# Optimization experiments

Hardware: AMD Instinct MI355X
Metric: run time of the kernel (lower is better)

## Reference

```python
import jax, jax.numpy as jnp
import numpy as np

N, E, G, D, C = 50000, 800000, 512, 128, 10
BN_EPS = 1e-5

def setup_inputs() -> dict:
    key = jax.random.key(0)
    ks = jax.random.split(key, 12)
    inp = {
        'x': jnp.zeros((N,), dtype=jnp.int64 if jax.config.jax_enable_x64 else jnp.int32),
        'edge_index': jax.random.randint(ks[0], (2, E), 0, N),
        'batch_ids': jnp.sort(jax.random.randint(ks[1], (N,), 0, G)),
        'emb': jax.random.normal(ks[2], (1, D), jnp.float32),
        'W1a': jax.random.normal(ks[3], (D, D), jnp.float32) * 0.05,
        'b1a': jnp.zeros((D,), jnp.float32),
        'g1': jnp.ones((D,), jnp.float32),
        'be1': jnp.zeros((D,), jnp.float32),
        'W1b': jax.random.normal(ks[4], (D, D), jnp.float32) * 0.05,
        'b1b': jnp.zeros((D,), jnp.float32),
        'W2a': jax.random.normal(ks[5], (D, D), jnp.float32) * 0.05,
        'b2a': jnp.zeros((D,), jnp.float32),
        'g2': jnp.ones((D,), jnp.float32),
        'be2': jnp.zeros((D,), jnp.float32),
        'W2b': jax.random.normal(ks[6], (D, D), jnp.float32) * 0.05,
        'b2b': jnp.zeros((D,), jnp.float32),
        'Wm': jax.random.normal(ks[7], (D, C), jnp.float32) * 0.05,
        'bm': jnp.zeros((C,), jnp.float32),
        'Wx': jax.random.normal(ks[8], (D, C), jnp.float32) * 0.05,
        'bx': jnp.zeros((C,), jnp.float32),
        'ens_w': jnp.array([0.6, 0.4], jnp.float32),
    }
    return inp

def _gin_layer(h, src, dst, Wa, ba, g, be, Wb, bb):
    # GINConv, eps=0: mlp(x + sum_{j in N(i)} x_j)
    agg = jax.ops.segment_sum(h[src], dst, num_segments=N)  # [N, D]
    z = (h + agg) @ Wa + ba
    mu = jnp.mean(z, axis=0)
    var = jnp.var(z, axis=0)  # biased, as torch BN training forward
    z = (z - mu) * jax.lax.rsqrt(var + BN_EPS) * g + be
    z = jax.nn.relu(z)  # dropout is identity in eval
    return z @ Wb + bb

def reference(x, edge_index, batch_ids, emb, W1a, b1a, g1, be1, W1b, b1b,
              W2a, b2a, g2, be2, W2b, b2b, Wm, bm, Wx, bx, ens_w):
    src, dst = edge_index[0], edge_index[1]
    h0 = emb[x]  # [N, D] (all indices 0)
    h1 = _gin_layer(h0, src, dst, W1a, b1a, g1, be1, W1b, b1b)
    h2 = _gin_layer(h1, src, dst, W2a, b2a, g2, be2, W2b, b2b) + h1
    # global mean / max pooling over batch segments
    counts = jax.ops.segment_sum(jnp.ones((N,), h2.dtype), batch_ids, num_segments=G)
    mean_repr = jax.ops.segment_sum(h2, batch_ids, num_segments=G) / jnp.maximum(counts, 1.0)[:, None]
    max_repr = jax.ops.segment_max(h2, batch_ids, num_segments=G)
    max_repr = jnp.where(jnp.isfinite(max_repr), max_repr, 0.0)  # empty segments -> 0
    logits_mean = mean_repr @ Wm + bm
    logits_max = max_repr @ Wx + bx
    w = jax.nn.softmax(ens_w)
    ensemble_logits = w[0] * logits_mean + w[1] * logits_max
    return (ensemble_logits, logits_mean, logits_max, (mean_repr, max_repr))
```

## Files before the change

### kernel.cpp

```cpp
#include <hip/hip_runtime.h>
#include <math.h>

#define N_NODES  50000
#define N_EDGES  800000
#define N_GRAPHS 512
#define DIM      128
#define NCLS     10
#define KH       64
#define KW       32
#define KT       128
#define OVF_CAP  65536
#define BN_EPS   1e-5f

#define TR       32
#define NB_GEMM  ((N_NODES + TR - 1) / TR)
#define NB_EDGE  ((N_EDGES / 4 + 255) / 256)
#define NB_MID   (NB_EDGE + KT)


__global__ void k_zero(uint4* __restrict__ p, int n4) {
    int i = blockIdx.x * blockDim.x + threadIdx.x;
    if (i < n4) p[i] = make_uint4(0u, 0u, 0u, 0u);
}

__global__ void k_count_deg(const int4* __restrict__ dst4, int* __restrict__ deg,
                            uint4* __restrict__ m4) {
    int e = blockIdx.x * blockDim.x + threadIdx.x;
    const uint4 z = make_uint4(0u, 0u, 0u, 0u);
    for (int i = e; i < N_NODES * KW / 4; i += NB_EDGE * 256) m4[i] = z;
    if (e < N_EDGES / 4) {
        int4 d = dst4[e];
        atomicAdd(&deg[d.x], 1);
        atomicAdd(&deg[d.y], 1);
        atomicAdd(&deg[d.z], 1);
        atomicAdd(&deg[d.w], 1);
    }
}

__device__ inline int lower_bound_i(const int* __restrict__ a, int n, int v) {
    int lo = 0, hi = n;
    while (lo < hi) {
        int mid = (lo + hi) >> 1;
        if (a[mid] < v) lo = mid + 1; else hi = mid;
    }
    return lo;
}

__global__ __launch_bounds__(256) void k_mid(
        const int4* __restrict__ src4, const int4* __restrict__ dst4,
        const int* __restrict__ deg, unsigned int* __restrict__ m,
        unsigned int* __restrict__ ovf_cnt, int* __restrict__ ovf_buf,
        const float* __restrict__ emb, const float* __restrict__ W1a,
        const float* __restrict__ g1, const float* __restrict__ be1,
        const float* __restrict__ W1b, const float* __restrict__ b1b,
        const float* __restrict__ W2a, const float* __restrict__ b2b,
        float* __restrict__ table, float* __restrict__ table2) {
    const int t = threadIdx.x;
    if ((int)blockIdx.x < NB_EDGE) {
        int e = blockIdx.x * 256 + t;
        if (e >= N_EDGES / 4) return;
        int4 sv = src4[e];
        int4 dv = dst4[e];
        int ss[4] = {sv.x, sv.y, sv.z, sv.w};
        int dd[4] = {dv.x, dv.y, dv.z, dv.w};
        #pragma unroll
        for (int j = 0; j < 4; ++j) {
            int k = deg[ss[j]];
            if (k < KH) {
                atomicAdd(&m[(size_t)dd[j] * KW + (k >> 1)], 1u << ((k & 1) << 4));
            } else {
                unsigned int idx = atomicAdd(ovf_cnt, 1u);
                if (idx < OVF_CAP) {
                    ovf_buf[2 * idx] = dd[j];
                    ovf_buf[2 * idx + 1] = k < KT ? k : KT - 1;
                }
            }
        }
    } else {
        __shared__ unsigned long long sred[256];
        __shared__ float r[DIM];
        __shared__ float traw[DIM];
        const int k = blockIdx.x - NB_EDGE;
        unsigned long long s = 0;
        for (int i = t; i < N_NODES; i += 256) {
            unsigned long long d = (unsigned long long)(unsigned int)deg[i];
            s += d * d;
        }
        sred[t] = s;
        __syncthreads();
        for (int st = 128; st > 0; st >>= 1) {
            if (t < st) sred[t] += sred[t + st];
            __syncthreads();
        }
        if (t < DIM) {
            float u = 0.f;
            for (int j = 0; j < DIM; ++j) u += emb[j] * W1a[j * DIM + t];
            double mdeg = (double)N_EDGES / (double)N_NODES;
            double vdeg = (double)sred[0] / (double)N_NODES - mdeg * mdeg;
            float var = (float)((double)u * (double)u * vdeg);
            float rs  = rsqrtf(var + BN_EPS);
            float A   = u * rs * g1[t];
            float B   = be1[t] - (float)mdeg * A;
            r[t] = fmaxf((float)k * A + B, 0.f);
        }
        __syncthreads();
        if (t < DIM) {
            float acc = b1b[t];
            for (int j = 0; j < DIM; ++j) acc += r[j] * W1b[j * DIM + t];
            traw[t] = acc;
            table[(size_t)k * DIM + t] = acc + b2b[t];
        }
        __syncthreads();
        if (t < DIM) {
            float acc2 = 0.f;
            for (int j = 0; j < DIM; ++j) acc2 += traw[j] * W2a[j * DIM + t];
            table2[(size_t)k * DIM + t] = acc2;
        }
    }
}

__global__ __launch_bounds__(256) void k_gemm1(
        const unsigned int* __restrict__ m, const int* __restrict__ deg,
        const float* __restrict__ table2, const float* __restrict__ b2a,
        float* __restrict__ z2, float* __restrict__ spart,
        const unsigned int* __restrict__ ovf_cnt, const int* __restrict__ ovf_buf) {
    __shared__ __align__(16) float nsh[TR * 68];
    const int t = threadIdx.x;
    const int i0 = blockIdx.x * TR;
    {
        int row = t >> 3, w4 = (t & 7) << 2;
        uint4 v = make_uint4(0u, 0u, 0u, 0u);
        if (i0 + row < N_NODES) v = *(const uint4*)&m[(size_t)(i0 + row) * KW + w4];
        float* np = &nsh[row * 68 + (w4 << 1)];
        float4 f0 = make_float4((float)(v.x & 0xFFFFu), (float)(v.x >> 16),
                                (float)(v.y & 0xFFFFu), (float)(v.y >> 16));
        float4 f1 = make_float4((float)(v.z & 0xFFFFu), (float)(v.z >> 16),
                                (float)(v.w & 0xFFFFu), (float)(v.w >> 16));
        *(float4*)&np[0] = f0;
        *(float4*)&np[4] = f1;
    }
    __syncthreads();
    if (t < TR) {
        int i = i0 + t;
        if (i < N_NODES) {
            int d = deg[i];
            if (d < KH) nsh[t * 68 + d] += 1.f;
        }
    }
    __syncthreads();

    const int g = t >> 5;
    const int c4 = (t & 31) << 2;
    const int rbase = g * 4;
    float acc[4][4] = {};
    #pragma unroll 2
    for (int kb = 0; kb < 16; ++kb) {
        const int k0 = kb * 4;
        float4 w0 = *(const float4*)&table2[(size_t)(k0 + 0) * DIM + c4];
        float4 w1 = *(const float4*)&table2[(size_t)(k0 + 1) * DIM + c4];
        float4 w2 = *(const float4*)&table2[(size_t)(k0 + 2) * DIM + c4];
        float4 w3 = *(const float4*)&table2[(size_t)(k0 + 3) * DIM + c4];
        #pragma unroll
        for (int r = 0; r < 4; ++r) {
            float4 nr = *(const float4*)&nsh[(rbase + r) * 68 + k0];
            acc[r][0] += nr.x * w0.x + nr.y * w1.x + nr.z * w2.x + nr.w * w3.x;
            acc[r][1] += nr.x * w0.y + nr.y * w1.y + nr.z * w2.y + nr.w * w3.y;
            acc[r][2] += nr.x * w0.z + nr.y * w1.z + nr.z * w2.z + nr.w * w3.z;
            acc[r][3] += nr.x * w0.w + nr.y * w1.w + nr.z * w2.w + nr.w * w3.w;
        }
    }

    unsigned int nov = *ovf_cnt;
    if (nov > OVF_CAP) nov = OVF_CAP;
    for (unsigned int u = 0; u < nov; ++u) {
        int dd = ovf_buf[2 * u];
        int rr = dd - i0;
        if (rr >= 0 && rr < TR && (rr >> 2) == g) {
            int kk = ovf_buf[2 * u + 1];
            float4 tv = *(const float4*)&table2[(size_t)kk * DIM + c4];
            acc[rr & 3][0] += tv.x; acc[rr & 3][1] += tv.y;
            acc[rr & 3][2] += tv.z; acc[rr & 3][3] += tv.w;
        }
    }

    float4 bb = *(const float4*)&b2a[c4];
    float s4[4] = {0.f, 0.f, 0.f, 0.f};
    float q4[4] = {0.f, 0.f, 0.f, 0.f};
    #pragma unroll
    for (int r = 0; r < 4; ++r) {
        int row = i0 + rbase + r;
        if (row < N_NODES) {
            float v0 = acc[r][0] + bb.x;
            float v1 = acc[r][1] + bb.y;
            float v2 = acc[r][2] + bb.z;
            float v3 = acc[r][3] + bb.w;
            int kk = deg[row];
            if (kk >= KH) {
                if (kk > KT - 1) kk = KT - 1;
                float4 sv = *(const float4*)&table2[(size_t)kk * DIM + c4];
                v0 += sv.x; v1 += sv.y; v2 += sv.z; v3 += sv.w;
            }
            *(float4*)&z2[(size_t)row * DIM + c4] = make_float4(v0, v1, v2, v3);
            s4[0] += v0; q4[0] += v0 * v0;
            s4[1] += v1; q4[1] += v1 * v1;
            s4[2] += v2; q4[2] += v2 * v2;
            s4[3] += v3; q4[3] += v3 * v3;
        }
    }
    __syncthreads();
    float* red = nsh;
    #pragma unroll
    for (int j = 0; j < 4; ++j) {
        red[g * 128 + c4 + j] = s4[j];
        red[1024 + g * 128 + c4 + j] = q4[j];
    }
    __syncthreads();
    if (t < 128) {
        float ss = 0.f, qq = 0.f;
        #pragma unroll
        for (int gg = 0; gg < 8; ++gg) {
            ss += red[gg * 128 + t];
            qq += red[1024 + gg * 128 + t];
        }
        spart[(size_t)blockIdx.x * 256 + t] = ss;
        spart[(size_t)blockIdx.x * 256 + 128 + t] = qq;
    }
}

__global__ __launch_bounds__(1024) void k_fin(
        const float* __restrict__ spart,
        const float* __restrict__ g2, const float* __restrict__ be2,
        float* __restrict__ A2, float* __restrict__ B2) {
    __shared__ double red[4 * 256];
    int t = threadIdx.x & 255;
    int q = threadIdx.x >> 8;
    double acc = 0.0;
    #pragma unroll 4
    for (int b = q; b < NB_GEMM; b += 4) acc += (double)spart[(size_t)b * 256 + t];
    red[q * 256 + t] = acc;
    __syncthreads();
    if (threadIdx.x < 256)
        red[threadIdx.x] = red[threadIdx.x] + red[256 + threadIdx.x] +
                           red[512 + threadIdx.x] + red[768 + threadIdx.x];
    __syncthreads();
    if (threadIdx.x < 128) {
        double mu = red[threadIdx.x] / (double)N_NODES;
        double var = red[128 + threadIdx.x] / (double)N_NODES - mu * mu;
        float rs = rsqrtf((float)var + BN_EPS);
        float a = rs * g2[threadIdx.x];
        A2[threadIdx.x] = a;
        B2[threadIdx.x] = be2[threadIdx.x] - (float)mu * a;
    }
}

__global__ __launch_bounds__(256) void k_gemm2(
        const float* __restrict__ z2, const float* __restrict__ A2,
        const float* __restrict__ B2, const float* __restrict__ W2b,
        const float* __restrict__ table, const int* __restrict__ deg,
        float* __restrict__ h2) {
    __shared__ __align__(16) float lds_zn[TR * 132];
    const int t = threadIdx.x;
    const int i0 = blockIdx.x * TR;
    #pragma unroll
    for (int q = 0; q < 4; ++q) {
        int idx = t + 256 * q;
        int row = idx >> 5, cc = (idx & 31) << 2;
        float4 zv = make_float4(0.f, 0.f, 0.f, 0.f);
        if (i0 + row < N_NODES) zv = *(const float4*)&z2[(size_t)(i0 + row) * DIM + cc];
        float4 av = *(const float4*)&A2[cc];
        float4 bv = *(const float4*)&B2[cc];
        lds_zn[row * 132 + cc + 0] = fmaxf(zv.x * av.x + bv.x, 0.f);
        lds_zn[row * 132 + cc + 1] = fmaxf(zv.y * av.y + bv.y, 0.f);
        lds_zn[row * 132 + cc + 2] = fmaxf(zv.z * av.z + bv.z, 0.f);
        lds_zn[row * 132 + cc + 3] = fmaxf(zv.w * av.w + bv.w, 0.f);
    }
    __syncthreads();

    const int g = t >> 5;
    const int c4 = (t & 31) << 2;
    const int rbase = g * 4;
    float acc[4][4] = {};
    #pragma unroll 2
    for (int kb = 0; kb < 32; ++kb) {
        const int k0 = kb * 4;
        float4 w0 = *(const float4*)&W2b[(size_t)(k0 + 0) * DIM + c4];
        float4 w1 = *(const float4*)&W2b[(size_t)(k0 + 1) * DIM + c4];
        float4 w2 = *(const float4*)&W2b[(size_t)(k0 + 2) * DIM + c4];
        float4 w3 = *(const float4*)&W2b[(size_t)(k0 + 3) * DIM + c4];
        #pragma unroll
        for (int r = 0; r < 4; ++r) {
            float4 zr = *(const float4*)&lds_zn[(rbase + r) * 132 + k0];
            acc[r][0] += zr.x * w0.x + zr.y * w1.x + zr.z * w2.x + zr.w * w3.x;
            acc[r][1] += zr.x * w0.y + zr.y * w1.y + zr.z * w2.y + zr.w * w3.y;
            acc[r][2] += zr.x * w0.z + zr.y * w1.z + zr.z * w2.z + zr.w * w3.z;
            acc[r][3] += zr.x * w0.w + zr.y * w1.w + zr.z * w2.w + zr.w * w3.w;
        }
    }

    #pragma unroll
    for (int r = 0; r < 4; ++r) {
        int row = i0 + rbase + r;
        if (row < N_NODES) {
            int kk = deg[row]; if (kk > KT - 1) kk = KT - 1;
            float4 tb = *(const float4*)&table[(size_t)kk * DIM + c4];
            float4 o;
            o.x = acc[r][0] + tb.x;
            o.y = acc[r][1] + tb.y;
            o.z = acc[r][2] + tb.z;
            o.w = acc[r][3] + tb.w;
            *(float4*)&h2[(size_t)row * DIM + c4] = o;
        }
    }
}

__global__ __launch_bounds__(1024) void k_poolhead(
        const float* __restrict__ h2, const int* __restrict__ batch,
        const float* __restrict__ Wm, const float* __restrict__ bm,
        const float* __restrict__ Wx, const float* __restrict__ bx,
        const float* __restrict__ ensw,
        float* __restrict__ out_ens, float* __restrict__ out_lm,
        float* __restrict__ out_lx,
        float* __restrict__ out_mean, float* __restrict__ out_max) {
    __shared__ float reds[32 * 132];
    __shared__ float redm[32 * 132];
    int g = blockIdx.x;
    int s0 = lower_bound_i(batch, N_NODES, g);
    int e0 = lower_bound_i(batch, N_NODES, g + 1);
    int rg = threadIdx.x >> 5;
    int c4 = (threadIdx.x & 31) << 2;
    float s[4] = {0.f, 0.f, 0.f, 0.f};
    float mx[4] = {-INFINITY, -INFINITY, -INFINITY, -INFINITY};
    for (int i = s0 + rg; i < e0; i += 32) {
        float4 v = *(const float4*)&h2[(size_t)i * DIM + c4];
        s[0] += v.x; mx[0] = fmaxf(mx[0], v.x);
        s[1] += v.y; mx[1] = fmaxf(mx[1], v.y);
        s[2] += v.z; mx[2] = fmaxf(mx[2], v.z);
        s[3] += v.w; mx[3] = fmaxf(mx[3], v.w);
    }
    #pragma unroll
    for (int j = 0; j < 4; ++j) {
        reds[rg * 132 + c4 + j] = s[j];
        redm[rg * 132 + c4 + j] = mx[j];
    }
    __syncthreads();
    for (int step = 16; step >= 1; step >>= 1) {
        if (rg < step) {
            #pragma unroll
            for (int j = 0; j < 4; ++j) {
                reds[rg * 132 + c4 + j] += reds[(rg + step) * 132 + c4 + j];
                redm[rg * 132 + c4 + j] = fmaxf(redm[rg * 132 + c4 + j],
                                                redm[(rg + step) * 132 + c4 + j]);
            }
        }
        __syncthreads();
    }
    if (rg == 0) {
        int cnt = e0 - s0;
        float denom = (float)(cnt > 0 ? cnt : 1);
        #pragma unroll
        for (int j = 0; j < 4; ++j) {
            float mean = reds[c4 + j] / denom;
            float mxv  = (cnt > 0) ? redm[c4 + j] : 0.f;
            out_mean[(size_t)g * DIM + c4 + j] = mean;
            out_max[(size_t)g * DIM + c4 + j]  = mxv;
            reds[c4 + j] = mean;
            redm[c4 + j] = mxv;
        }
    }
    __syncthreads();
    int t = threadIdx.x;
    if (t < NCLS) {
        float lm = bm[t], lx = bx[t];
        for (int d = 0; d < DIM; ++d) {
            lm += reds[d] * Wm[d * NCLS + t];
            lx += redm[d] * Wx[d * NCLS + t];
        }
        float a0 = ensw[0], a1 = ensw[1];
        float mw = fmaxf(a0, a1);
        float e0v = expf(a0 - mw), e1v = expf(a1 - mw);
        float inv = 1.f / (e0v + e1v);
        out_lm[(size_t)g * NCLS + t] = lm;
        out_lx[(size_t)g * NCLS + t] = lx;
        out_ens[(size_t)g * NCLS + t] = (e0v * inv) * lm + (e1v * inv) * lx;
    }
}


extern "C" void kernel_launch(void* const* d_in, const int* in_sizes, int n_in,
                              void* d_out, int out_size, void* d_ws, size_t ws_size,
                              hipStream_t stream) {
    const int* edge = (const int*)d_in[1];
    const int* src = edge;
    const int* dst = edge + N_EDGES;
    const int* batch = (const int*)d_in[2];
    const float* emb = (const float*)d_in[3];
    const float* W1a = (const float*)d_in[4];
    const float* g1  = (const float*)d_in[6];
    const float* be1 = (const float*)d_in[7];
    const float* W1b = (const float*)d_in[8];
    const float* b1b = (const float*)d_in[9];
    const float* W2a = (const float*)d_in[10];
    const float* b2a = (const float*)d_in[11];
    const float* g2  = (const float*)d_in[12];
    const float* be2 = (const float*)d_in[13];
    const float* W2b = (const float*)d_in[14];
    const float* b2b = (const float*)d_in[15];
    const float* Wm  = (const float*)d_in[16];
    const float* bm  = (const float*)d_in[17];
    const float* Wx  = (const float*)d_in[18];
    const float* bx  = (const float*)d_in[19];
    const float* ensw = (const float*)d_in[20];

    char* ws = (char*)d_ws;
    size_t off = 0;
    auto take = [&](size_t bytes) {
        char* p = ws + off;
        off += (bytes + 511) & ~(size_t)511;
        return p;
    };
    int* deg                  = (int*)take((size_t)N_NODES * 4);
    unsigned int* ovf_cnt     = (unsigned int*)take(4);
    size_t zbytes = off;
    unsigned int* m           = (unsigned int*)take((size_t)N_NODES * KW * 4);
    float* spart              = (float*)take((size_t)NB_GEMM * 256 * 4);
    int* ovf_buf              = (int*)take((size_t)OVF_CAP * 2 * 4);
    float* table              = (float*)take((size_t)KT * DIM * 4);
    float* table2             = (float*)take((size_t)KT * DIM * 4);
    float* A2                 = (float*)take(DIM * 4);
    float* B2                 = (float*)take(DIM * 4);
    float* z2                 = (float*)take((size_t)N_NODES * DIM * 4);
    float* h2                 = (float*)take((size_t)N_NODES * DIM * 4);
    (void)ws_size; (void)in_sizes; (void)n_in; (void)out_size;

    float* out      = (float*)d_out;
    float* out_ens  = out;
    float* out_lm   = out + (size_t)N_GRAPHS * NCLS;
    float* out_lx   = out + 2 * (size_t)N_GRAPHS * NCLS;
    float* out_mean = out + 3 * (size_t)N_GRAPHS * NCLS;
    float* out_max  = out_mean + (size_t)N_GRAPHS * DIM;

    int n4 = (int)(zbytes >> 4);
    k_zero<<<(n4 + 255) / 256, 256, 0, stream>>>((uint4*)ws, n4);
    k_count_deg<<<NB_EDGE, 256, 0, stream>>>((const int4*)dst, deg, (uint4*)m);
    k_mid<<<NB_MID, 256, 0, stream>>>((const int4*)src, (const int4*)dst, deg, m,
                                      ovf_cnt, ovf_buf, emb, W1a, g1, be1,
                                      W1b, b1b, W2a, b2b, table, table2);
    k_gemm1<<<NB_GEMM, 256, 0, stream>>>(m, deg, table2, b2a, z2, spart,
                                         ovf_cnt, ovf_buf);
    k_fin<<<1, 1024, 0, stream>>>(spart, g2, be2, A2, B2);
    k_gemm2<<<NB_GEMM, 256, 0, stream>>>(z2, A2, B2, W2b, table, deg, h2);
    k_poolhead<<<N_GRAPHS, 1024, 0, stream>>>(h2, batch, Wm, bm, Wx, bx, ensw,
                                              out_ens, out_lm, out_lx, out_mean, out_max);
}
```

Measured before the change: 217.2 us.

## Replicate degree and neighbor-degree histograms across copies to cut atomic contention

Degree counting and the per-node neighbor-degree histogram now go into NCOPY replicated arrays, chosen by block index, to spread atomic contention. The histogram counters shrink from 16-bit to 8-bit, with nodes of degree above 255 sent to the overflow path. A new merge kernel sums the degree copies and computes per-block sums of squared degrees, so k_mid's 128 table blocks no longer each rescan all degrees. gemm1 sums the 8 histogram copies on load, and h2 aliases z2 to save workspace, which adds memory traffic to zero and read as well as one more kernel launch.

After: 201.4 us. -7.3%, faster.

```diff
diff --git a/kernel.cpp b/kernel.cpp
--- a/kernel.cpp
+++ b/kernel.cpp
@@ -7,15 +7,17 @@
 #define DIM      128
 #define NCLS     10
 #define KH       64
-#define KW       32
 #define KT       128
 #define OVF_CAP  65536
 #define BN_EPS   1e-5f
+#define NCOPY    8
 
 #define TR       32
 #define NB_GEMM  ((N_NODES + TR - 1) / TR)
 #define NB_EDGE  ((N_EDGES / 4 + 255) / 256)
 #define NB_MID   (NB_EDGE + KT)
+#define NB_DEGM  ((N_NODES + 255) / 256)
+#define M8_WORDS ((size_t)NCOPY * N_NODES * 16)
 
 
 __global__ void k_zero(uint4* __restrict__ p, int n4) {
@@ -23,18 +25,42 @@
     if (i < n4) p[i] = make_uint4(0u, 0u, 0u, 0u);
 }
 
-__global__ void k_count_deg(const int4* __restrict__ dst4, int* __restrict__ deg,
-                            uint4* __restrict__ m4) {
+__global__ void k_count_deg(const int4* __restrict__ dst4, int* __restrict__ deg8,
+                            uint4* __restrict__ m84) {
     int e = blockIdx.x * blockDim.x + threadIdx.x;
     const uint4 z = make_uint4(0u, 0u, 0u, 0u);
-    for (int i = e; i < N_NODES * KW / 4; i += NB_EDGE * 256) m4[i] = z;
+    for (size_t i = e; i < M8_WORDS / 4; i += (size_t)NB_EDGE * 256) m84[i] = z;
     if (e < N_EDGES / 4) {
-        int4 d = dst4[e];
-        atomicAdd(&deg[d.x], 1);
-        atomicAdd(&deg[d.y], 1);
-        atomicAdd(&deg[d.z], 1);
-        atomicAdd(&deg[d.w], 1);
-    }
+        int* d = deg8 + (size_t)(blockIdx.x & (NCOPY - 1)) * N_NODES;
+        int4 v = dst4[e];
+        atomicAdd(&d[v.x], 1);
+        atomicAdd(&d[v.y], 1);
+        atomicAdd(&d[v.z], 1);
+        atomicAdd(&d[v.w], 1);
+    }
+}
+
+__global__ __launch_bounds__(256) void k_degmerge(
+        const int* __restrict__ deg8, int* __restrict__ deg,
+        unsigned long long* __restrict__ dpart) {
+    __shared__ unsigned long long red[256];
+    const int t = threadIdx.x;
+    int i = blockIdx.x * 256 + t;
+    unsigned long long q = 0;
+    if (i < N_NODES) {
+        int s = 0;
+        #pragma unroll
+        for (int c = 0; c < NCOPY; ++c) s += deg8[(size_t)c * N_NODES + i];
+        deg[i] = s;
+        q = (unsigned long long)(unsigned int)s * (unsigned int)s;
+    }
+    red[t] = q;
+    __syncthreads();
+    for (int st = 128; st > 0; st >>= 1) {
+        if (t < st) red[t] += red[t + st];
+        __syncthreads();
+    }
+    if (t == 0) dpart[blockIdx.x] = red[0];
 }
 
 __device__ inline int lower_bound_i(const int* __restrict__ a, int n, int v) {
@@ -48,8 +74,9 @@
 
 __global__ __launch_bounds__(256) void k_mid(
         const int4* __restrict__ src4, const int4* __restrict__ dst4,
-        const int* __restrict__ deg, unsigned int* __restrict__ m,
+        const int* __restrict__ deg, unsigned int* __restrict__ m8,
         unsigned int* __restrict__ ovf_cnt, int* __restrict__ ovf_buf,
+        const unsigned long long* __restrict__ dpart,
         const float* __restrict__ emb, const float* __restrict__ W1a,
         const float* __restrict__ g1, const float* __restrict__ be1,
         const float* __restrict__ W1b, const float* __restrict__ b1b,
@@ -59,6 +86,7 @@
     if ((int)blockIdx.x < NB_EDGE) {
         int e = blockIdx.x * 256 + t;
         if (e >= N_EDGES / 4) return;
+        unsigned int* mc = m8 + (size_t)(blockIdx.x & (NCOPY - 1)) * N_NODES * 16;
         int4 sv = src4[e];
         int4 dv = dst4[e];
         int ss[4] = {sv.x, sv.y, sv.z, sv.w};
@@ -66,8 +94,9 @@
         #pragma unroll
         for (int j = 0; j < 4; ++j) {
             int k = deg[ss[j]];
-            if (k < KH) {
-                atomicAdd(&m[(size_t)dd[j] * KW + (k >> 1)], 1u << ((k & 1) << 4));
+            int dn = deg[dd[j]];
+            if (k < KH && dn <= 255) {
+                atomicAdd(&mc[(size_t)dd[j] * 16 + (k >> 2)], 1u << ((k & 3) << 3));
             } else {
                 unsigned int idx = atomicAdd(ovf_cnt, 1u);
                 if (idx < OVF_CAP) {
@@ -81,11 +110,7 @@
         __shared__ float r[DIM];
         __shared__ float traw[DIM];
         const int k = blockIdx.x - NB_EDGE;
-        unsigned long long s = 0;
-        for (int i = t; i < N_NODES; i += 256) {
-            unsigned long long d = (unsigned long long)(unsigned int)deg[i];
-            s += d * d;
-        }
+        unsigned long long s = (t < NB_DEGM) ? dpart[t] : 0ull;
         sred[t] = s;
         __syncthreads();
         for (int st = 128; st > 0; st >>= 1) {
@@ -120,7 +145,7 @@
 }
 
 __global__ __launch_bounds__(256) void k_gemm1(
-        const unsigned int* __restrict__ m, const int* __restrict__ deg,
+        const unsigned int* __restrict__ m8, const int* __restrict__ deg,
         const float* __restrict__ table2, const float* __restrict__ b2a,
         float* __restrict__ z2, float* __restrict__ spart,
         const unsigned int* __restrict__ ovf_cnt, const int* __restrict__ ovf_buf) {
@@ -128,16 +153,28 @@
     const int t = threadIdx.x;
     const int i0 = blockIdx.x * TR;
     {
-        int row = t >> 3, w4 = (t & 7) << 2;
-        uint4 v = make_uint4(0u, 0u, 0u, 0u);
-        if (i0 + row < N_NODES) v = *(const uint4*)&m[(size_t)(i0 + row) * KW + w4];
-        float* np = &nsh[row * 68 + (w4 << 1)];
-        float4 f0 = make_float4((float)(v.x & 0xFFFFu), (float)(v.x >> 16),
-                                (float)(v.y & 0xFFFFu), (float)(v.y >> 16));
-        float4 f1 = make_float4((float)(v.z & 0xFFFFu), (float)(v.z >> 16),
-                                (float)(v.w & 0xFFFFu), (float)(v.w >> 16));
-        *(float4*)&np[0] = f0;
-        *(float4*)&np[4] = f1;
+        int node = t >> 3;
+        int wg = (t & 7) << 1;
+        int gi = i0 + node;
+        float f0 = 0.f, f1 = 0.f, f2 = 0.f, f3 = 0.f;
+        float f4 = 0.f, f5 = 0.f, f6 = 0.f, f7 = 0.f;
+        if (gi < N_NODES) {
+            #pragma unroll
+            for (int c = 0; c < NCOPY; ++c) {
+                uint2 v = *(const uint2*)&m8[((size_t)c * N_NODES + gi) * 16 + wg];
+                f0 += (float)(v.x & 0xFFu);
+                f1 += (float)((v.x >> 8) & 0xFFu);
+                f2 += (float)((v.x >> 16) & 0xFFu);
+                f3 += (float)(v.x >> 24);
+                f4 += (float)(v.y & 0xFFu);
+                f5 += (float)((v.y >> 8) & 0xFFu);
+                f6 += (float)((v.y >> 16) & 0xFFu);
+                f7 += (float)(v.y >> 24);
+            }
+        }
+        float* np = &nsh[node * 68 + (wg << 2)];
+        np[0] = f0; np[1] = f1; np[2] = f2; np[3] = f3;
+        np[4] = f4; np[5] = f5; np[6] = f6; np[7] = f7;
     }
     __syncthreads();
     if (t < TR) {
@@ -254,10 +291,10 @@
 }
 
 __global__ __launch_bounds__(256) void k_gemm2(
-        const float* __restrict__ z2, const float* __restrict__ A2,
+        const float* z2, const float* __restrict__ A2,
         const float* __restrict__ B2, const float* __restrict__ W2b,
         const float* __restrict__ table, const int* __restrict__ deg,
-        float* __restrict__ h2) {
+        float* h2) {
     __shared__ __align__(16) float lds_zn[TR * 132];
     const int t = threadIdx.x;
     const int i0 = blockIdx.x * TR;
@@ -418,10 +455,12 @@
         off += (bytes + 511) & ~(size_t)511;
         return p;
     };
-    int* deg                  = (int*)take((size_t)N_NODES * 4);
+    int* deg8                 = (int*)take((size_t)NCOPY * N_NODES * 4);
     unsigned int* ovf_cnt     = (unsigned int*)take(4);
     size_t zbytes = off;
-    unsigned int* m           = (unsigned int*)take((size_t)N_NODES * KW * 4);
+    int* deg                  = (int*)take((size_t)N_NODES * 4);
+    unsigned int* m8          = (unsigned int*)take(M8_WORDS * 4);
+    unsigned long long* dpart = (unsigned long long*)take((size_t)NB_DEGM * 8);
     float* spart              = (float*)take((size_t)NB_GEMM * 256 * 4);
     int* ovf_buf              = (int*)take((size_t)OVF_CAP * 2 * 4);
     float* table              = (float*)take((size_t)KT * DIM * 4);
@@ -429,7 +468,7 @@
     float* A2                 = (float*)take(DIM * 4);
     float* B2                 = (float*)take(DIM * 4);
     float* z2                 = (float*)take((size_t)N_NODES * DIM * 4);
-    float* h2                 = (float*)take((size_t)N_NODES * DIM * 4);
+    float* h2                 = z2;
     (void)ws_size; (void)in_sizes; (void)n_in; (void)out_size;
 
     float* out      = (float*)d_out;
@@ -441,11 +480,12 @@
 
     int n4 = (int)(zbytes >> 4);
     k_zero<<<(n4 + 255) / 256, 256, 0, stream>>>((uint4*)ws, n4);
-    k_count_deg<<<NB_EDGE, 256, 0, stream>>>((const int4*)dst, deg, (uint4*)m);
-    k_mid<<<NB_MID, 256, 0, stream>>>((const int4*)src, (const int4*)dst, deg, m,
-                                      ovf_cnt, ovf_buf, emb, W1a, g1, be1,
+    k_count_deg<<<NB_EDGE, 256, 0, stream>>>((const int4*)dst, deg8, (uint4*)m8);
+    k_degmerge<<<NB_DEGM, 256, 0, stream>>>(deg8, deg, dpart);
+    k_mid<<<NB_MID, 256, 0, stream>>>((const int4*)src, (const int4*)dst, deg, m8,
+                                      ovf_cnt, ovf_buf, dpart, emb, W1a, g1, be1,
                                       W1b, b1b, W2a, b2b, table, table2);
-    k_gemm1<<<NB_GEMM, 256, 0, stream>>>(m, deg, table2, b2a, z2, spart,
+    k_gemm1<<<NB_GEMM, 256, 0, stream>>>(m8, deg, table2, b2a, z2, spart,
                                          ovf_cnt, ovf_buf);
     k_fin<<<1, 1024, 0, stream>>>(spart, g2, be2, A2, B2);
     k_gemm2<<<NB_GEMM, 256, 0, stream>>>(z2, A2, B2, W2b, table, deg, h2);
```
